# Kernel optimization log

Measured on AMD Instinct MI355X. Metric: run time of the kernel, lower is better.

## Reference

```python
import jax, jax.numpy as jnp
import numpy as np

D, H, DH = 768, 12, 64
W = 256            # one-sided window (attention_window=512 total)
EPS = 1e-6
NEG = -1e9


def layer_norm(x, g, b):
    m = jnp.mean(x, axis=-1, keepdims=True)
    v = jnp.mean((x - m) ** 2, axis=-1, keepdims=True)
    return g * (x - m) * jax.lax.rsqrt(v + EPS) + b


def _blocks3(t, nb):
    # t: [B,H,nb,W,dh] -> keys/values of 3 neighboring blocks [B,H,nb,3W,dh]
    tp = jnp.pad(t, ((0, 0), (0, 0), (1, 1), (0, 0), (0, 0)))
    return jnp.concatenate([tp[:, :, :nb], tp[:, :, 1:nb + 1], tp[:, :, 2:nb + 2]], axis=3)


def sliding_window_attention(x, kpm, Wq, bq, Wk, bk, Wv, bv, Wo, bo):
    B, S, _ = x.shape
    nb = S // W
    def proj(Wm, bm):
        return (x @ Wm + bm).reshape(B, S, H, DH).transpose(0, 2, 1, 3).reshape(B, H, nb, W, DH)
    q = proj(Wq, bq) * (1.0 / np.sqrt(DH))
    k = proj(Wk, bk)
    v = proj(Wv, bv)
    k3 = _blocks3(k, nb)
    v3 = _blocks3(v, nb)
    # scores over local band: [B,H,nb,W,3W]
    s = jnp.einsum('bhnqd,bhnkd->bhnqk', q, k3)
    qi = jnp.arange(W)[:, None]
    kj = jnp.arange(3 * W)[None, :]
    band = jnp.abs(kj - W - qi) <= W                     # [W,3W]
    kg = (jnp.arange(nb)[:, None, None] - 1) * W + kj[None]  # global key idx [nb,1,3W]
    inrange = (kg >= 0) & (kg < S)
    # key padding mask gathered into block layout: [B,nb,3W]
    kpm_b = jnp.pad(kpm.reshape(B, nb, W), ((0, 0), (1, 1), (0, 0)), constant_values=True)
    kpm3 = jnp.concatenate([kpm_b[:, :nb], kpm_b[:, 1:nb + 1], kpm_b[:, 2:nb + 2]], axis=2)
    m = band[None, None, None] & inrange[None, None] & (~kpm3)[:, None, :, None, :]
    s = jnp.where(m, s, NEG)
    p = jax.nn.softmax(s, axis=-1)
    o = jnp.einsum('bhnqk,bhnkd->bhnqd', p, v3)
    o = o.reshape(B, H, S, DH).transpose(0, 2, 1, 3).reshape(B, S, D)
    return o @ Wo + bo


def setup_inputs() -> dict:
    key = jax.random.key(0)
    ks = jax.random.split(key, 12)
    B, S, DF = 2, 4096, 3072
    sc = 1.0 / np.sqrt(D)
    return {
        'x': jax.random.normal(ks[0], (B, S, D), jnp.float32),
        'mask': jnp.zeros((B, S), bool),
        'id': 0,
        'Wq': jax.random.normal(ks[1], (D, D), jnp.float32) * sc,
        'bq': jnp.zeros((D,), jnp.float32),
        'Wk': jax.random.normal(ks[2], (D, D), jnp.float32) * sc,
        'bk': jnp.zeros((D,), jnp.float32),
        'Wv': jax.random.normal(ks[3], (D, D), jnp.float32) * sc,
        'bv': jnp.zeros((D,), jnp.float32),
        'Wo': jax.random.normal(ks[4], (D, D), jnp.float32) * sc,
        'bo': jnp.zeros((D,), jnp.float32),
        'ln1_g': jnp.ones((D,), jnp.float32),
        'ln1_b': jnp.zeros((D,), jnp.float32),
        'W1': jax.random.normal(ks[5], (D, DF), jnp.float32) * sc,
        'b1': jnp.zeros((DF,), jnp.float32),
        'W2': jax.random.normal(ks[6], (DF, D), jnp.float32) * (1.0 / np.sqrt(DF)),
        'b2': jnp.zeros((D,), jnp.float32),
        'ln2_g': jnp.ones((D,), jnp.float32),
        'ln2_b': jnp.zeros((D,), jnp.float32),
    }


def reference(x, mask, id, Wq, bq, Wk, bk, Wv, bv, Wo, bo, ln1_g, ln1_b, W1, b1, W2, b2, ln2_g, ln2_b):
    # Sublayer 1: pre-norm residual around sliding-window self-attention
    h = layer_norm(x, ln1_g, ln1_b)
    x = x + sliding_window_attention(h, mask, Wq, bq, Wk, bk, Wv, bv, Wo, bo)
    # Sublayer 2: pre-norm residual around positionwise FFN
    h = layer_norm(x, ln2_g, ln2_b)
    x = x + (jax.nn.relu(h @ W1 + b1) @ W2 + b2)
    return x
```

## Files before the change

### kernel.cpp

```cpp
#include <hip/hip_runtime.h>
#include <hip/hip_bf16.h>
#include <cstddef>

typedef __attribute__((ext_vector_type(8))) short short8;
typedef __attribute__((ext_vector_type(4))) float f32x4;
typedef __attribute__((ext_vector_type(4))) unsigned short us4;

typedef __attribute__((address_space(1))) void as1_void;
typedef __attribute__((address_space(3))) void as3_void;

__device__ __forceinline__ void gload16(const void* g, void* lds) {
  __builtin_amdgcn_global_load_lds((as1_void*)(void*)g, (as3_void*)lds, 16, 0, 0);
}

__device__ inline unsigned short f2bf(float f) {
  union { float f; unsigned int u; } v; v.f = f;
  return (unsigned short)((v.u + 0x7FFFu + ((v.u >> 16) & 1u)) >> 16);
}

__device__ __forceinline__ float exp2v(float x) {
  float r; asm("v_exp_f32 %0, %1" : "=v"(r) : "v"(x)); return r;
}
__device__ __forceinline__ unsigned cvtpk(float a, float b) {
  unsigned r; asm("v_cvt_pk_bf16_f32 %0, %1, %2" : "=v"(r) : "v"(a), "v"(b)); return r;
}

__global__ __launch_bounds__(256) void ln_kernel(const float* __restrict__ x,
    const float* __restrict__ g, const float* __restrict__ b,
    unsigned short* __restrict__ out)
{
  int row = blockIdx.x, t = threadIdx.x;
  const float* xr = x + (size_t)row * 768;
  float v0 = xr[t], v1 = xr[t + 256], v2 = xr[t + 512];
  float s = v0 + v1 + v2;
  #pragma unroll
  for (int o = 32; o > 0; o >>= 1) s += __shfl_xor(s, o);
  __shared__ float r1[4], r2[4];
  if ((t & 63) == 0) r1[t >> 6] = s;
  __syncthreads();
  float mean = (r1[0] + r1[1] + r1[2] + r1[3]) * (1.0f / 768.0f);
  float d0 = v0 - mean, d1 = v1 - mean, d2 = v2 - mean;
  float q = d0 * d0 + d1 * d1 + d2 * d2;
  #pragma unroll
  for (int o = 32; o > 0; o >>= 1) q += __shfl_xor(q, o);
  if ((t & 63) == 0) r2[t >> 6] = q;
  __syncthreads();
  float var = (r2[0] + r2[1] + r2[2] + r2[3]) * (1.0f / 768.0f);
  float rs = rsqrtf(var + 1e-6f);
  unsigned short* orow = out + (size_t)row * 768;
  orow[t]       = f2bf(g[t]       * d0 * rs + b[t]);
  orow[t + 256] = f2bf(g[t + 256] * d1 * rs + b[t + 256]);
  orow[t + 512] = f2bf(g[t + 512] * d2 * rs + b[t + 512]);
}

__global__ __launch_bounds__(256) void prep_kernel(
    const float* __restrict__ Wq, const float* __restrict__ Wk,
    const float* __restrict__ Wv, const float* __restrict__ Wo,
    const float* __restrict__ W1, const float* __restrict__ W2,
    const float* __restrict__ bq, const float* __restrict__ bk,
    const float* __restrict__ bv,
    unsigned short* __restrict__ WTqkv, unsigned short* __restrict__ WTo,
    unsigned short* __restrict__ W1T, unsigned short* __restrict__ W2T,
    float* __restrict__ bqkv)
{
  int bid = blockIdx.x;
  if (bid >= 6912) {
    int i = (bid - 6912) * 256 + threadIdx.x;
    bqkv[i] = (i < 768) ? bq[i] : ((i < 1536) ? bk[i - 768] : bv[i - 1536]);
    return;
  }
  const float* W; unsigned short* WT; int K, N, lb;
  if (bid < 576)       { W = Wq; WT = WTqkv;                        K = 768;  N = 768;  lb = bid; }
  else if (bid < 1152) { W = Wk; WT = WTqkv + (size_t)768 * 768;    K = 768;  N = 768;  lb = bid - 576; }
  else if (bid < 1728) { W = Wv; WT = WTqkv + (size_t)1536 * 768;   K = 768;  N = 768;  lb = bid - 1152; }
  else if (bid < 2304) { W = Wo; WT = WTo;                          K = 768;  N = 768;  lb = bid - 1728; }
  else if (bid < 4608) { W = W1; WT = W1T;                          K = 768;  N = 3072; lb = bid - 2304; }
  else                 { W = W2; WT = W2T;                          K = 3072; N = 768;  lb = bid - 4608; }
  int ntN = N >> 5;
  int k0 = (lb / ntN) * 32, n0 = (lb % ntN) * 32;
  __shared__ float tile[32][33];
  int tx = threadIdx.x & 31, ty = threadIdx.x >> 5;
  #pragma unroll
  for (int i = 0; i < 32; i += 8)
    tile[ty + i][tx] = W[(size_t)(k0 + ty + i) * N + n0 + tx];
  __syncthreads();
  #pragma unroll
  for (int i = 0; i < 32; i += 8)
    WT[(size_t)(n0 + ty + i) * K + k0 + tx] = f2bf(tile[tx][ty + i]);
}

enum { EPI_QKV = 0, EPI_RELU = 1, EPI_RESID = 2 };

template<int EPI>
__global__ __launch_bounds__(512, 1) void gemmP_kernel(
    const unsigned short* __restrict__ A, const unsigned short* __restrict__ BT,
    const float* __restrict__ bias, const float* __restrict__ resid,
    void* __restrict__ outp, int M, int N, int K, int ntn)
{
  __shared__ char lds[3][49152];
  int tid = threadIdx.x;
  int nwg = gridDim.x;
  int bid = ((int)blockIdx.x & 7) * (nwg >> 3) + ((int)blockIdx.x >> 3);
  int mt = bid / ntn, nt = bid % ntn;
  int m0 = mt * 128, n0 = nt * 256;
  int w = tid >> 6, l = tid & 63;
  int wr = w >> 2, wc = w & 3;
  int fr = l & 15, fq = l >> 4;
  int swz = (fr >> 1) * 128 + (((((fr & 1) << 2) | fq) ^ ((fr >> 1) & 7)) << 4);
  int t8 = tid >> 3;
  int uu = (tid & 7) ^ (t8 & 7);
  int rb = 2 * t8 + (uu >> 2);
  int kb = (uu & 3) * 8;
  const unsigned short* Asrc  = A  + (size_t)(m0 + rb) * K + kb;
  const unsigned short* Bsrc0 = BT + (size_t)(n0 + rb) * K + kb;
  const unsigned short* Bsrc1 = BT + (size_t)(n0 + 128 + rb) * K + kb;

  auto stage = [&](int buf, int kt, int h) {
    int ko = kt * 64 + h * 32;
    char* dA = &lds[buf][0] + h * 8192 + (w << 10);
    char* dB = &lds[buf][16384] + h * 16384 + (w << 10);
    gload16(Asrc + ko, dA);
    gload16(Bsrc0 + ko, dB);
    gload16(Bsrc1 + ko, dB + 8192);
  };

  f32x4 acc[4][4] = {};
  short8 af[4], bf[4];

#define GP_READ(RBUF, H)                                                       \
  { const char* ab_ = &lds[RBUF][0] + (H) * 8192 + wr * 4096 + swz;            \
    const char* bb_ = &lds[RBUF][16384] + (H) * 16384 + wc * 4096 + swz;       \
    _Pragma("unroll")                                                          \
    for (int i_ = 0; i_ < 4; i_++) af[i_] = *(const short8*)(ab_ + i_ * 1024); \
    _Pragma("unroll")                                                          \
    for (int j_ = 0; j_ < 4; j_++) bf[j_] = *(const short8*)(bb_ + j_ * 1024); }

#define GP_MFMA                                                                \
  __builtin_amdgcn_s_setprio(1);                                               \
  _Pragma("unroll")                                                            \
  for (int i_ = 0; i_ < 4; i_++)                                               \
    _Pragma("unroll")                                                          \
    for (int j_ = 0; j_ < 4; j_++)                                             \
      acc[i_][j_] = __builtin_amdgcn_mfma_f32_16x16x32_bf16(                   \
          af[i_], bf[j_], acc[i_][j_], 0, 0, 0);                               \
  __builtin_amdgcn_s_setprio(0);

#define GP_PHASE(VN, RBUF, H, DOSTAGE, WBUF, KT)                               \
  asm volatile("s_waitcnt vmcnt(" #VN ")" ::: "memory");                       \
  __builtin_amdgcn_s_barrier();                                                \
  GP_READ(RBUF, H);                                                            \
  if (DOSTAGE) stage(WBUF, KT, H);                                             \
  asm volatile("" ::: "memory");                                               \
  __builtin_amdgcn_s_barrier();                                                \
  GP_MFMA;

  stage(0, 0, 0); stage(0, 0, 1); stage(1, 1, 0); stage(1, 1, 1);

  int NT = K >> 6;
  int R = 0;
  for (int t = 0; t < NT - 2; ++t) {
    int W = (R == 0) ? 2 : R - 1;
    GP_PHASE(9, R, 0, 1, W, t + 2);
    GP_PHASE(9, R, 1, 1, W, t + 2);
    R = (R == 2) ? 0 : R + 1;
  }
  GP_PHASE(9, R, 0, 0, 0, 0);
  GP_PHASE(6, R, 1, 0, 0, 0);
  R = (R == 2) ? 0 : R + 1;
  GP_PHASE(3, R, 0, 0, 0, 0);
  GP_PHASE(0, R, 1, 0, 0, 0);
#undef GP_PHASE
#undef GP_MFMA
#undef GP_READ

  #pragma unroll
  for (int nj = 0; nj < 4; nj++) {
    int col = n0 + wc * 64 + nj * 16 + fr;
    float bs = bias[col];
    if (EPI == EPI_QKV) {
      int which = (col >= 1536) ? 2 : ((col >= 768) ? 1 : 0);
      int c2 = col - which * 768;
      int hh = c2 >> 6, dh = c2 & 63;
      if (which == 2) {
        unsigned short* dstv = reinterpret_cast<unsigned short*>(outp) + (size_t)2 * 8192 * 768;
        #pragma unroll
        for (int i = 0; i < 4; i++) {
          int row0 = m0 + wr * 64 + i * 16 + fq * 4;
          int bb = row0 >> 12, sl = row0 & 4095;
          us4 pv;
          #pragma unroll
          for (int r = 0; r < 4; r++) pv[r] = f2bf(acc[i][nj][r] + bs);
          *reinterpret_cast<us4*>(&dstv[((size_t)(bb * 12 + hh) * 64 + dh) * 4096 + sl]) = pv;
        }
      } else {
        unsigned short* dst = reinterpret_cast<unsigned short*>(outp) + (size_t)which * 8192 * 768;
        #pragma unroll
        for (int i = 0; i < 4; i++) {
          #pragma unroll
          for (int r = 0; r < 4; r++) {
            int row = m0 + wr * 64 + i * 16 + fq * 4 + r;
            float c = acc[i][nj][r] + bs;
            if (which == 0) c *= 0.18033688011112042f;
            int bb = row >> 12, sl = row & 4095;
            dst[(((size_t)(bb * 12 + hh)) * 4096 + sl) * 64 + dh] = f2bf(c);
          }
        }
      }
    } else if (EPI == EPI_RELU) {
      #pragma unroll
      for (int i = 0; i < 4; i++)
        #pragma unroll
        for (int r = 0; r < 4; r++) {
          int row = m0 + wr * 64 + i * 16 + fq * 4 + r;
          float c = fmaxf(acc[i][nj][r] + bs, 0.0f);
          reinterpret_cast<unsigned short*>(outp)[(size_t)row * N + col] = f2bf(c);
        }
    } else {
      #pragma unroll
      for (int i = 0; i < 4; i++)
        #pragma unroll
        for (int r = 0; r < 4; r++) {
          int row = m0 + wr * 64 + i * 16 + fq * 4 + r;
          float c = acc[i][nj][r] + bs + resid[(size_t)row * N + col];
          reinterpret_cast<float*>(outp)[(size_t)row * N + col] = c;
        }
    }
  }
}

__global__ __launch_bounds__(256) void attn_fused_kernel(
    const unsigned short* __restrict__ qg, const unsigned short* __restrict__ kg,
    const unsigned short* __restrict__ vtg, const unsigned char* __restrict__ kpm,
    unsigned short* __restrict__ attn_out)
{
  __shared__ unsigned short lds_k[3][64 * 64];
  __shared__ unsigned short lds_vt[3][64 * 64];
  __shared__ unsigned short lds_p[4][32 * 64];
  int bid0 = blockIdx.x;
  int bid = (bid0 & 7) * 96 + (bid0 >> 3);
  int qblk = bid & 31, h = (bid >> 5) % 12, b = bid / 384;
  int bh = b * 12 + h;
  int q0 = qblk * 128;
  int tid = threadIdx.x, w = tid >> 6, l = tid & 63;
  int fr = l & 15, fq = l >> 4;
  int qw0 = q0 + w * 32;
  int swzb = (((l & 7) ^ (l >> 3)) << 4);
  const char* qbase  = (const char*)(qg  + (size_t)bh * 4096 * 64);
  const char* kbase  = (const char*)(kg  + (size_t)bh * 4096 * 64);
  const char* vtbase = (const char*)(vtg + (size_t)bh * 64 * 4096);
  const unsigned char* kpmb = kpm + (size_t)b * 4096;

  #pragma unroll
  for (int s = 0; s < 4; s++) {
    int row = w * 32 + s * 8 + (l >> 3);
    gload16(qbase + (size_t)(q0 + row) * 128 + swzb, (char*)lds_p[w] + s * 1024);
  }

  auto stageKV = [&](int c, int buf) {
    int g0 = q0 - 256 + c * 64;
    if (g0 < 0 || g0 >= 4096) return;
    #pragma unroll
    for (int s = 0; s < 2; s++) {
      int row = w * 16 + s * 8 + (l >> 3);
      gload16(kbase + (size_t)(g0 + row) * 128 + swzb,
              (char*)lds_k[buf] + (w * 2 + s) * 1024);
      gload16(vtbase + ((size_t)row * 4096 + g0) * 2 + swzb,
              (char*)lds_vt[buf] + (w * 2 + s) * 1024);
    }
  };
  auto stageKVc = [&](int c, int buf) {
    int g0 = q0 - 256 + c * 64;
    g0 = (g0 < 0) ? 0 : ((g0 > 4032) ? 4032 : g0);
    #pragma unroll
    for (int s = 0; s < 2; s++) {
      int row = w * 16 + s * 8 + (l >> 3);
      gload16(kbase + (size_t)(g0 + row) * 128 + swzb,
              (char*)lds_k[buf] + (w * 2 + s) * 1024);
      gload16(vtbase + ((size_t)row * 4096 + g0) * 2 + swzb,
              (char*)lds_vt[buf] + (w * 2 + s) * 1024);
    }
  };
  (void)stageKV;

  stageKVc(0, 0);
  stageKVc(1, 1);
  asm volatile("s_waitcnt vmcnt(8)" ::: "memory");

  short8 qf[2][2];
  #pragma unroll
  for (int i = 0; i < 2; i++)
    #pragma unroll
    for (int ks = 0; ks < 2; ks++)
      qf[i][ks] = *(const short8*)((const char*)lds_p[w] + (i * 16 + fr) * 128 +
                    ((ks * 64 + fq * 16) ^ ((fr & 7) << 4)));

  f32x4 acc_o[2][4] = {};
  float m_st[2] = {-3.0e38f, -3.0e38f};
  float l_st[2] = {0.0f, 0.0f};

  for (int c = 0; c < 10; c++) {
    if (c < 9) { asm volatile("s_waitcnt vmcnt(4)" ::: "memory"); }
    else       { asm volatile("s_waitcnt vmcnt(0)" ::: "memory"); }
    __builtin_amdgcn_s_barrier();
    if (c < 8) stageKVc(c + 2, (c + 2) % 3);
    int g0 = q0 - 256 + c * 64;
    bool valid = (g0 >= 0) && (g0 < 4096);
    if (valid) {
      int buf = c % 3;
      unsigned int km[4];
      #pragma unroll
      for (int j = 0; j < 4; j++)
        km[j] = *(const unsigned int*)(kpmb + g0 + 16 * j + 4 * fq);
      bool anyk = __any((km[0] | km[1] | km[2] | km[3]) != 0);
      int rel = g0 - qw0;
      bool edge = anyk || (rel < -225) || (rel > 193);
      short8 kf[4][2];
      #pragma unroll
      for (int j = 0; j < 4; j++)
        #pragma unroll
        for (int ks = 0; ks < 2; ks++)
          kf[j][ks] = *(const short8*)((const char*)lds_k[buf] + (j * 16 + fr) * 128 +
                        ((ks * 64 + fq * 16) ^ ((fr & 7) << 4)));
      f32x4 accs[4][2] = {};
      #pragma unroll
      for (int j = 0; j < 4; j++)
        #pragma unroll
        for (int i = 0; i < 2; i++)
          #pragma unroll
          for (int ks = 0; ks < 2; ks++)
            accs[j][i] = __builtin_amdgcn_mfma_f32_16x16x32_bf16(kf[j][ks], qf[i][ks], accs[j][i], 0, 0, 0);
      #pragma unroll
      for (int i = 0; i < 2; i++) {
        float sv[4][4];
        #pragma unroll
        for (int j = 0; j < 4; j++)
          #pragma unroll
          for (int r = 0; r < 4; r++)
            sv[j][r] = accs[j][i][r];
        if (edge) {
          int base = rel + 4 * fq - fr - 16 * i;
          #pragma unroll
          for (int j = 0; j < 4; j++)
            #pragma unroll
            for (int r = 0; r < 4; r++) {
              int d = base + 16 * j + r;
              bool ok = (d >= -256) && (d <= 256) && (((km[j] >> (8 * r)) & 255u) == 0u);
              if (!ok) sv[j][r] = -1.0e9f;
            }
        }
        float mv = sv[0][0];
        #pragma unroll
        for (int j = 0; j < 4; j++)
          #pragma unroll
          for (int r = 0; r < 4; r++) mv = fmaxf(mv, sv[j][r]);
        mv = fmaxf(mv, __shfl_xor(mv, 16));
        mv = fmaxf(mv, __shfl_xor(mv, 32));
        float mo = m_st[i];
        if (!__all(mv - mo <= 8.0f)) {
          float mn = fmaxf(mo, mv);
          float scl = exp2v(mo - mn);
          l_st[i] *= scl;
          m_st[i] = mn;
          #pragma unroll
          for (int r = 0; r < 4; r++) {
            float so = __shfl(scl, (l & 48) | ((l >> 2) & 12) | r);
            #pragma unroll
            for (int jd = 0; jd < 4; jd++) acc_o[i][jd][r] *= so;
          }
        }
        float mn = m_st[i];
        float rs = 0.0f;
        char* prow = (char*)lds_p[w] + (i * 16 + fr) * 128;
        #pragma unroll
        for (int j = 0; j < 4; j++) {
          float p0 = exp2v(sv[j][0] - mn), p1 = exp2v(sv[j][1] - mn);
          float p2 = exp2v(sv[j][2] - mn), p3 = exp2v(sv[j][3] - mn);
          rs += (p0 + p1) + (p2 + p3);
          uint2 u; u.x = cvtpk(p0, p1); u.y = cvtpk(p2, p3);
          *(uint2*)(prow + ((32 * j + 8 * fq) ^ ((fr & 7) << 4))) = u;
        }
        rs += __shfl_xor(rs, 16);
        rs += __shfl_xor(rs, 32);
        l_st[i] += rs;
      }
      short8 pf[2][2];
      #pragma unroll
      for (int i = 0; i < 2; i++)
        #pragma unroll
        for (int ks = 0; ks < 2; ks++)
          pf[i][ks] = *(const short8*)((const char*)lds_p[w] + (i * 16 + fr) * 128 +
                        ((ks * 64 + fq * 16) ^ ((fr & 7) << 4)));
      short8 vf[4][2];
      #pragma unroll
      for (int jd = 0; jd < 4; jd++)
        #pragma unroll
        for (int ks = 0; ks < 2; ks++)
          vf[jd][ks] = *(const short8*)((const char*)lds_vt[buf] + (jd * 16 + fr) * 128 +
                        ((ks * 64 + fq * 16) ^ ((fr & 7) << 4)));
      #pragma unroll
      for (int i = 0; i < 2; i++)
        #pragma unroll
        for (int jd = 0; jd < 4; jd++)
          #pragma unroll
          for (int ks = 0; ks < 2; ks++)
            acc_o[i][jd] = __builtin_amdgcn_mfma_f32_16x16x32_bf16(pf[i][ks], vf[jd][ks], acc_o[i][jd], 0, 0, 0);
    }
  }
  #pragma unroll
  for (int i = 0; i < 2; i++) {
    #pragma unroll
    for (int r = 0; r < 4; r++) {
      float lv = __shfl(l_st[i], (l & 48) | ((l >> 2) & 12) | r);
      float inv = 1.0f / lv;
      int qrow = qw0 + i * 16 + fq * 4 + r;
      size_t orow = ((size_t)b * 4096 + qrow) * 768 + h * 64;
      #pragma unroll
      for (int jd = 0; jd < 4; jd++)
        attn_out[orow + jd * 16 + fr] = f2bf(acc_o[i][jd][r] * inv);
    }
  }
}

extern "C" void kernel_launch(void* const* d_in, const int* in_sizes, int n_in,
                              void* d_out, int out_size, void* d_ws, size_t ws_size,
                              hipStream_t stream) {
  const float* x            = (const float*)d_in[0];
  const unsigned char* mask = (const unsigned char*)d_in[1];
  const float* Wq  = (const float*)d_in[3];
  const float* bq  = (const float*)d_in[4];
  const float* Wk  = (const float*)d_in[5];
  const float* bk  = (const float*)d_in[6];
  const float* Wv  = (const float*)d_in[7];
  const float* bv  = (const float*)d_in[8];
  const float* Wo  = (const float*)d_in[9];
  const float* bo  = (const float*)d_in[10];
  const float* ln1g = (const float*)d_in[11];
  const float* ln1b = (const float*)d_in[12];
  const float* W1  = (const float*)d_in[13];
  const float* b1  = (const float*)d_in[14];
  const float* W2  = (const float*)d_in[15];
  const float* b2  = (const float*)d_in[16];
  const float* ln2g = (const float*)d_in[17];
  const float* ln2b = (const float*)d_in[18];
  float* out = (float*)d_out;

  char* ws = (char*)d_ws;
  size_t off = 0;
  auto alloc = [&](size_t bytes) -> void* {
    void* p = ws + off;
    off += (bytes + 255) & ~(size_t)255;
    return p;
  };
  unsigned short* WTqkv = (unsigned short*)alloc((size_t)2304 * 768 * 2);
  unsigned short* WTo   = (unsigned short*)alloc((size_t)768 * 768 * 2);
  unsigned short* W1T   = (unsigned short*)alloc((size_t)3072 * 768 * 2);
  unsigned short* W2T   = (unsigned short*)alloc((size_t)768 * 3072 * 2);
  float*          bqkv  = (float*)alloc(2304 * 4);
  unsigned short* hbuf  = (unsigned short*)alloc((size_t)8192 * 768 * 2);
  unsigned short* qkv   = (unsigned short*)alloc((size_t)3 * 8192 * 768 * 2);
  unsigned short* attn  = (unsigned short*)alloc((size_t)8192 * 768 * 2);
  float* x1             = (float*)alloc((size_t)8192 * 768 * 4);
  unsigned short* h2    = (unsigned short*)alloc((size_t)8192 * 768 * 2);
  unsigned short* a1    = (unsigned short*)alloc((size_t)8192 * 3072 * 2);

  prep_kernel<<<6921, 256, 0, stream>>>(Wq, Wk, Wv, Wo, W1, W2, bq, bk, bv,
                                        WTqkv, WTo, W1T, W2T, bqkv);

  ln_kernel<<<8192, 256, 0, stream>>>(x, ln1g, ln1b, hbuf);

  gemmP_kernel<EPI_QKV><<<576, 512, 0, stream>>>(hbuf, WTqkv, bqkv, nullptr, qkv, 8192, 2304, 768, 9);

  attn_fused_kernel<<<768, 256, 0, stream>>>(qkv, qkv + (size_t)8192 * 768,
                                             qkv + (size_t)2 * 8192 * 768, mask, attn);

  gemmP_kernel<EPI_RESID><<<192, 512, 0, stream>>>(attn, WTo, bo, x, x1, 8192, 768, 768, 3);
  ln_kernel<<<8192, 256, 0, stream>>>(x1, ln2g, ln2b, h2);
  gemmP_kernel<EPI_RELU><<<768, 512, 0, stream>>>(h2, W1T, b1, nullptr, a1, 8192, 3072, 768, 12);
  gemmP_kernel<EPI_RESID><<<192, 512, 0, stream>>>(a1, W2T, b2, x1, out, 8192, 768, 3072, 3);
}
```

Baseline: 259.4 us.

## Replace GEMM with 64x256 double-buffered 4-wave kernel and fold LN1 into prep

Replaces the 128x256 triple-buffered 8-wave GEMM with a 64x256 tile, 256-thread, double-buffered kernel that allows two blocks per CU and launches twice as many workgroups. The first layer norm is merged into the weight-prep kernel as extra blocks, which removes one launch. The unused bounds-checked KV staging lambda is also dropped. Each block now reuses B data over fewer rows, and the simpler pipeline waits on all loads and a full barrier every K step, which could expose more memory latency.

```diff
diff --git a/kernel.cpp b/kernel.cpp
--- a/kernel.cpp
+++ b/kernel.cpp
@@ -61,11 +61,39 @@
     const float* __restrict__ bv,
     unsigned short* __restrict__ WTqkv, unsigned short* __restrict__ WTo,
     unsigned short* __restrict__ W1T, unsigned short* __restrict__ W2T,
-    float* __restrict__ bqkv)
+    float* __restrict__ bqkv,
+    const float* __restrict__ x, const float* __restrict__ ln1g,
+    const float* __restrict__ ln1b, unsigned short* __restrict__ hbuf)
 {
   int bid = blockIdx.x;
+  int t = threadIdx.x;
+  if (bid >= 6921) {
+    int row = bid - 6921;
+    const float* xr = x + (size_t)row * 768;
+    float v0 = xr[t], v1 = xr[t + 256], v2 = xr[t + 512];
+    float s = v0 + v1 + v2;
+    #pragma unroll
+    for (int o = 32; o > 0; o >>= 1) s += __shfl_xor(s, o);
+    __shared__ float r1[4], r2[4];
+    if ((t & 63) == 0) r1[t >> 6] = s;
+    __syncthreads();
+    float mean = (r1[0] + r1[1] + r1[2] + r1[3]) * (1.0f / 768.0f);
+    float d0 = v0 - mean, d1 = v1 - mean, d2 = v2 - mean;
+    float q = d0 * d0 + d1 * d1 + d2 * d2;
+    #pragma unroll
+    for (int o = 32; o > 0; o >>= 1) q += __shfl_xor(q, o);
+    if ((t & 63) == 0) r2[t >> 6] = q;
+    __syncthreads();
+    float var = (r2[0] + r2[1] + r2[2] + r2[3]) * (1.0f / 768.0f);
+    float rs = rsqrtf(var + 1e-6f);
+    unsigned short* orow = hbuf + (size_t)row * 768;
+    orow[t]       = f2bf(ln1g[t]       * d0 * rs + ln1b[t]);
+    orow[t + 256] = f2bf(ln1g[t + 256] * d1 * rs + ln1b[t + 256]);
+    orow[t + 512] = f2bf(ln1g[t + 512] * d2 * rs + ln1b[t + 512]);
+    return;
+  }
   if (bid >= 6912) {
-    int i = (bid - 6912) * 256 + threadIdx.x;
+    int i = (bid - 6912) * 256 + t;
     bqkv[i] = (i < 768) ? bq[i] : ((i < 1536) ? bk[i - 768] : bv[i - 1536]);
     return;
   }
@@ -79,7 +107,7 @@
   int ntN = N >> 5;
   int k0 = (lb / ntN) * 32, n0 = (lb % ntN) * 32;
   __shared__ float tile[32][33];
-  int tx = threadIdx.x & 31, ty = threadIdx.x >> 5;
+  int tx = t & 31, ty = t >> 5;
   #pragma unroll
   for (int i = 0; i < 32; i += 8)
     tile[ty + i][tx] = W[(size_t)(k0 + ty + i) * N + n0 + tx];
@@ -92,90 +120,69 @@
 enum { EPI_QKV = 0, EPI_RELU = 1, EPI_RESID = 2 };
 
 template<int EPI>
-__global__ __launch_bounds__(512, 1) void gemmP_kernel(
+__global__ __launch_bounds__(256, 2) void gemmW_kernel(
     const unsigned short* __restrict__ A, const unsigned short* __restrict__ BT,
     const float* __restrict__ bias, const float* __restrict__ resid,
     void* __restrict__ outp, int M, int N, int K, int ntn)
 {
-  __shared__ char lds[3][49152];
+  __shared__ char lds[2][40960];
   int tid = threadIdx.x;
   int nwg = gridDim.x;
   int bid = ((int)blockIdx.x & 7) * (nwg >> 3) + ((int)blockIdx.x >> 3);
   int mt = bid / ntn, nt = bid % ntn;
-  int m0 = mt * 128, n0 = nt * 256;
+  int m0 = mt * 64, n0 = nt * 256;
   int w = tid >> 6, l = tid & 63;
-  int wr = w >> 2, wc = w & 3;
   int fr = l & 15, fq = l >> 4;
-  int swz = (fr >> 1) * 128 + (((((fr & 1) << 2) | fq) ^ ((fr >> 1) & 7)) << 4);
-  int t8 = tid >> 3;
-  int uu = (tid & 7) ^ (t8 & 7);
-  int rb = 2 * t8 + (uu >> 2);
-  int kb = (uu & 3) * 8;
-  const unsigned short* Asrc  = A  + (size_t)(m0 + rb) * K + kb;
-  const unsigned short* Bsrc0 = BT + (size_t)(n0 + rb) * K + kb;
-  const unsigned short* Bsrc1 = BT + (size_t)(n0 + 128 + rb) * K + kb;
-
-  auto stage = [&](int buf, int kt, int h) {
-    int ko = kt * 64 + h * 32;
-    char* dA = &lds[buf][0] + h * 8192 + (w << 10);
-    char* dB = &lds[buf][16384] + h * 16384 + (w << 10);
-    gload16(Asrc + ko, dA);
-    gload16(Bsrc0 + ko, dB);
-    gload16(Bsrc1 + ko, dB + 8192);
+  int rb = tid >> 3;
+  int sw8 = ((tid & 7) ^ (rb & 7)) * 8;
+  const unsigned short* As = A  + (size_t)(m0 + rb) * K + sw8;
+  const unsigned short* Bs = BT + (size_t)(n0 + rb) * K + sw8;
+
+  auto stage = [&](int buf, int kt) {
+    char* d = &lds[buf][0] + tid * 16;
+    #pragma unroll
+    for (int c = 0; c < 2; c++)
+      gload16(As + (size_t)(c * 32) * K + kt * 64, d + c * 4096);
+    #pragma unroll
+    for (int c = 0; c < 8; c++)
+      gload16(Bs + (size_t)(c * 32) * K + kt * 64, d + 8192 + c * 4096);
   };
 
   f32x4 acc[4][4] = {};
-  short8 af[4], bf[4];
-
-#define GP_READ(RBUF, H)                                                       \
-  { const char* ab_ = &lds[RBUF][0] + (H) * 8192 + wr * 4096 + swz;            \
-    const char* bb_ = &lds[RBUF][16384] + (H) * 16384 + wc * 4096 + swz;       \
-    _Pragma("unroll")                                                          \
-    for (int i_ = 0; i_ < 4; i_++) af[i_] = *(const short8*)(ab_ + i_ * 1024); \
-    _Pragma("unroll")                                                          \
-    for (int j_ = 0; j_ < 4; j_++) bf[j_] = *(const short8*)(bb_ + j_ * 1024); }
-
-#define GP_MFMA                                                                \
-  __builtin_amdgcn_s_setprio(1);                                               \
-  _Pragma("unroll")                                                            \
-  for (int i_ = 0; i_ < 4; i_++)                                               \
-    _Pragma("unroll")                                                          \
-    for (int j_ = 0; j_ < 4; j_++)                                             \
-      acc[i_][j_] = __builtin_amdgcn_mfma_f32_16x16x32_bf16(                   \
-          af[i_], bf[j_], acc[i_][j_], 0, 0, 0);                               \
-  __builtin_amdgcn_s_setprio(0);
-
-#define GP_PHASE(VN, RBUF, H, DOSTAGE, WBUF, KT)                               \
-  asm volatile("s_waitcnt vmcnt(" #VN ")" ::: "memory");                       \
-  __builtin_amdgcn_s_barrier();                                                \
-  GP_READ(RBUF, H);                                                            \
-  if (DOSTAGE) stage(WBUF, KT, H);                                             \
-  asm volatile("" ::: "memory");                                               \
-  __builtin_amdgcn_s_barrier();                                                \
-  GP_MFMA;
-
-  stage(0, 0, 0); stage(0, 0, 1); stage(1, 1, 0); stage(1, 1, 1);
+  stage(0, 0);
+  asm volatile("s_waitcnt vmcnt(0)" ::: "memory");
+  __syncthreads();
 
   int NT = K >> 6;
-  int R = 0;
-  for (int t = 0; t < NT - 2; ++t) {
-    int W = (R == 0) ? 2 : R - 1;
-    GP_PHASE(9, R, 0, 1, W, t + 2);
-    GP_PHASE(9, R, 1, 1, W, t + 2);
-    R = (R == 2) ? 0 : R + 1;
-  }
-  GP_PHASE(9, R, 0, 0, 0, 0);
-  GP_PHASE(6, R, 1, 0, 0, 0);
-  R = (R == 2) ? 0 : R + 1;
-  GP_PHASE(3, R, 0, 0, 0, 0);
-  GP_PHASE(0, R, 1, 0, 0, 0);
-#undef GP_PHASE
-#undef GP_MFMA
-#undef GP_READ
+  for (int t = 0; t < NT; ++t) {
+    int R = t & 1;
+    if (t + 1 < NT) stage(R ^ 1, t + 1);
+    #pragma unroll
+    for (int h = 0; h < 2; h++) {
+      short8 af[4], bf[4];
+      const char* base = &lds[R][0];
+      int colb = (h * 64 + fq * 16) ^ ((fr & 7) << 4);
+      #pragma unroll
+      for (int i = 0; i < 4; i++)
+        af[i] = *(const short8*)(base + (i * 16 + fr) * 128 + colb);
+      #pragma unroll
+      for (int j = 0; j < 4; j++)
+        bf[j] = *(const short8*)(base + 8192 + (w * 64 + j * 16 + fr) * 128 + colb);
+      __builtin_amdgcn_s_setprio(1);
+      #pragma unroll
+      for (int i = 0; i < 4; i++)
+        #pragma unroll
+        for (int j = 0; j < 4; j++)
+          acc[i][j] = __builtin_amdgcn_mfma_f32_16x16x32_bf16(af[i], bf[j], acc[i][j], 0, 0, 0);
+      __builtin_amdgcn_s_setprio(0);
+    }
+    asm volatile("s_waitcnt vmcnt(0)" ::: "memory");
+    __syncthreads();
+  }
 
   #pragma unroll
   for (int nj = 0; nj < 4; nj++) {
-    int col = n0 + wc * 64 + nj * 16 + fr;
+    int col = n0 + w * 64 + nj * 16 + fr;
     float bs = bias[col];
     if (EPI == EPI_QKV) {
       int which = (col >= 1536) ? 2 : ((col >= 768) ? 1 : 0);
@@ -185,7 +192,7 @@
         unsigned short* dstv = reinterpret_cast<unsigned short*>(outp) + (size_t)2 * 8192 * 768;
         #pragma unroll
         for (int i = 0; i < 4; i++) {
-          int row0 = m0 + wr * 64 + i * 16 + fq * 4;
+          int row0 = m0 + i * 16 + fq * 4;
           int bb = row0 >> 12, sl = row0 & 4095;
           us4 pv;
           #pragma unroll
@@ -198,7 +205,7 @@
         for (int i = 0; i < 4; i++) {
           #pragma unroll
           for (int r = 0; r < 4; r++) {
-            int row = m0 + wr * 64 + i * 16 + fq * 4 + r;
+            int row = m0 + i * 16 + fq * 4 + r;
             float c = acc[i][nj][r] + bs;
             if (which == 0) c *= 0.18033688011112042f;
             int bb = row >> 12, sl = row & 4095;
@@ -211,7 +218,7 @@
       for (int i = 0; i < 4; i++)
         #pragma unroll
         for (int r = 0; r < 4; r++) {
-          int row = m0 + wr * 64 + i * 16 + fq * 4 + r;
+          int row = m0 + i * 16 + fq * 4 + r;
           float c = fmaxf(acc[i][nj][r] + bs, 0.0f);
           reinterpret_cast<unsigned short*>(outp)[(size_t)row * N + col] = f2bf(c);
         }
@@ -220,7 +227,7 @@
       for (int i = 0; i < 4; i++)
         #pragma unroll
         for (int r = 0; r < 4; r++) {
-          int row = m0 + wr * 64 + i * 16 + fq * 4 + r;
+          int row = m0 + i * 16 + fq * 4 + r;
           float c = acc[i][nj][r] + bs + resid[(size_t)row * N + col];
           reinterpret_cast<float*>(outp)[(size_t)row * N + col] = c;
         }
@@ -256,9 +263,9 @@
     gload16(qbase + (size_t)(q0 + row) * 128 + swzb, (char*)lds_p[w] + s * 1024);
   }
 
-  auto stageKV = [&](int c, int buf) {
+  auto stageKVc = [&](int c, int buf) {
     int g0 = q0 - 256 + c * 64;
-    if (g0 < 0 || g0 >= 4096) return;
+    g0 = (g0 < 0) ? 0 : ((g0 > 4032) ? 4032 : g0);
     #pragma unroll
     for (int s = 0; s < 2; s++) {
       int row = w * 16 + s * 8 + (l >> 3);
@@ -268,19 +275,6 @@
               (char*)lds_vt[buf] + (w * 2 + s) * 1024);
     }
   };
-  auto stageKVc = [&](int c, int buf) {
-    int g0 = q0 - 256 + c * 64;
-    g0 = (g0 < 0) ? 0 : ((g0 > 4032) ? 4032 : g0);
-    #pragma unroll
-    for (int s = 0; s < 2; s++) {
-      int row = w * 16 + s * 8 + (l >> 3);
-      gload16(kbase + (size_t)(g0 + row) * 128 + swzb,
-              (char*)lds_k[buf] + (w * 2 + s) * 1024);
-      gload16(vtbase + ((size_t)row * 4096 + g0) * 2 + swzb,
-              (char*)lds_vt[buf] + (w * 2 + s) * 1024);
-    }
-  };
-  (void)stageKV;
 
   stageKVc(0, 0);
   stageKVc(1, 1);
@@ -463,18 +457,17 @@
   unsigned short* h2    = (unsigned short*)alloc((size_t)8192 * 768 * 2);
   unsigned short* a1    = (unsigned short*)alloc((size_t)8192 * 3072 * 2);
 
-  prep_kernel<<<6921, 256, 0, stream>>>(Wq, Wk, Wv, Wo, W1, W2, bq, bk, bv,
-                                        WTqkv, WTo, W1T, W2T, bqkv);
-
-  ln_kernel<<<8192, 256, 0, stream>>>(x, ln1g, ln1b, hbuf);
-
-  gemmP_kernel<EPI_QKV><<<576, 512, 0, stream>>>(hbuf, WTqkv, bqkv, nullptr, qkv, 8192, 2304, 768, 9);
+  prep_kernel<<<15113, 256, 0, stream>>>(Wq, Wk, Wv, Wo, W1, W2, bq, bk, bv,
+                                         WTqkv, WTo, W1T, W2T, bqkv,
+                                         x, ln1g, ln1b, hbuf);
+
+  gemmW_kernel<EPI_QKV><<<1152, 256, 0, stream>>>(hbuf, WTqkv, bqkv, nullptr, qkv, 8192, 2304, 768, 9);
 
   attn_fused_kernel<<<768, 256, 0, stream>>>(qkv, qkv + (size_t)8192 * 768,
                                              qkv + (size_t)2 * 8192 * 768, mask, attn);
 
-  gemmP_kernel<EPI_RESID><<<192, 512, 0, stream>>>(attn, WTo, bo, x, x1, 8192, 768, 768, 3);
+  gemmW_kernel<EPI_RESID><<<384, 256, 0, stream>>>(attn, WTo, bo, x, x1, 8192, 768, 768, 3);
   ln_kernel<<<8192, 256, 0, stream>>>(x1, ln2g, ln2b, h2);
-  gemmP_kernel<EPI_RELU><<<768, 512, 0, stream>>>(h2, W1T, b1, nullptr, a1, 8192, 3072, 768, 12);
-  gemmP_kernel<EPI_RESID><<<192, 512, 0, stream>>>(a1, W2T, b2, x1, out, 8192, 768, 3072, 3);
-}
+  gemmW_kernel<EPI_RELU><<<1536, 256, 0, stream>>>(h2, W1T, b1, nullptr, a1, 8192, 3072, 768, 12);
+  gemmW_kernel<EPI_RESID><<<384, 256, 0, stream>>>(a1, W2T, b2, x1, out, 8192, 768, 3072, 3);
+}
```

New measurement: 244.1 us. 1.06x faster.
